# Kernel tuning notes

Hardware: AMD Instinct MI355X
Metric: run time of the kernel (lower is better)

## Reference

```python
import jax, jax.numpy as jnp
import numpy as np

N_NODES = 100000
N_EDGES = 600000
DIM = 128
LN_EPS = 1e-5


def setup_inputs() -> dict:
    key = jax.random.key(0)
    ks = jax.random.split(key, 12)
    s = 1.0 / np.sqrt(DIM)
    return {
        "h": jax.random.normal(ks[0], (N_NODES, DIM), dtype=jnp.float32),
        "edge_src": jax.random.randint(ks[1], (N_EDGES,), 0, N_NODES, dtype=jnp.int32),
        "edge_dst": jax.random.randint(ks[2], (N_EDGES,), 0, N_NODES, dtype=jnp.int32),
        "W_self": jax.random.uniform(ks[3], (DIM, DIM), jnp.float32, -s, s),
        "b_self": jax.random.uniform(ks[4], (DIM,), jnp.float32, -s, s),
        "W_neigh": jax.random.uniform(ks[5], (DIM, DIM), jnp.float32, -s, s),
        "b_neigh": jax.random.uniform(ks[6], (DIM,), jnp.float32, -s, s),
        "W_gate": jax.random.uniform(ks[7], (DIM, 2 * DIM), jnp.float32, -s, s),
        "b_gate": jax.random.uniform(ks[8], (DIM,), jnp.float32, -s, s),
        "ln_gamma": jnp.ones((DIM,), jnp.float32),
        "ln_beta": jnp.zeros((DIM,), jnp.float32),
    }


def reference(h, edge_src, edge_dst, W_self, b_self, W_neigh, b_neigh, W_gate, b_gate, ln_gamma, ln_beta):
    n = h.shape[0]
    # self transform: [N, D]
    hs = h @ W_self.T + b_self
    # mean over predecessors via segment sum over edges (src -> dst)
    neigh_sum = jax.ops.segment_sum(h[edge_src], edge_dst, num_segments=n)
    counts = jax.ops.segment_sum(jnp.ones((edge_src.shape[0],), h.dtype), edge_dst, num_segments=n)
    has_pred = (counts > 0).astype(h.dtype)[:, None]
    neigh_mean = neigh_sum / jnp.maximum(counts, 1.0)[:, None]
    hn = neigh_mean @ W_neigh.T + b_neigh
    # nodes with no predecessors skip the neighbor term entirely (incl. bias)
    m = hs + has_pred * hn
    gate = jax.nn.sigmoid(jnp.concatenate([h, m], axis=-1) @ W_gate.T + b_gate)
    v = gate * m + (1.0 - gate) * h
    # LayerNorm (biased variance, as torch) + relu
    mu = jnp.mean(v, axis=-1, keepdims=True)
    var = jnp.mean(jnp.square(v - mu), axis=-1, keepdims=True)
    out = (v - mu) * jax.lax.rsqrt(var + LN_EPS) * ln_gamma + ln_beta
    return jax.nn.relu(out)
```

## Files before the change

kernel.cpp:

```cpp
#include <hip/hip_runtime.h>
#include <math.h>

#define N_NODES 100000
#define N_EDGES 600000
#define DIM 128
#define LN_EPS 1e-5f
#define SCAN_NBLK ((N_NODES + 255) / 256)
#define NTILES ((N_NODES + 127) / 128)
#define NODE_GRID 256

typedef __bf16 bf16x8 __attribute__((ext_vector_type(8)));
typedef __bf16 bf16x4 __attribute__((ext_vector_type(4)));
typedef float f32x4 __attribute__((ext_vector_type(4)));

__global__ __launch_bounds__(256)
void prep_kernel(const float* __restrict__ h, const int* __restrict__ edst,
                 __bf16* __restrict__ h_bf, int* __restrict__ counts) {
  int i = blockIdx.x * 256 + threadIdx.x;
  {
    const float4 v0 = *reinterpret_cast<const float4*>(h + (size_t)i * 8);
    const float4 v1 = *reinterpret_cast<const float4*>(h + (size_t)i * 8 + 4);
    bf16x8 b;
    b[0] = (__bf16)v0.x; b[1] = (__bf16)v0.y; b[2] = (__bf16)v0.z; b[3] = (__bf16)v0.w;
    b[4] = (__bf16)v1.x; b[5] = (__bf16)v1.y; b[6] = (__bf16)v1.z; b[7] = (__bf16)v1.w;
    *reinterpret_cast<bf16x8*>(h_bf + (size_t)i * 8) = b;
  }
  if (i < N_EDGES) atomicAdd(&counts[edst[i]], 1);
}

__global__ __launch_bounds__(256)
void scan1_kernel(const int* __restrict__ counts, int* __restrict__ block_sums) {
  int i = blockIdx.x * 256 + threadIdx.x;
  int v = (i < N_NODES) ? counts[i] : 0;
#pragma unroll
  for (int off = 1; off < 64; off <<= 1) v += __shfl_xor(v, off);
  __shared__ int ws[4];
  if ((threadIdx.x & 63) == 0) ws[threadIdx.x >> 6] = v;
  __syncthreads();
  if (threadIdx.x == 0) block_sums[blockIdx.x] = ws[0] + ws[1] + ws[2] + ws[3];
}

__global__ __launch_bounds__(256)
void scan3_kernel(const int* __restrict__ counts, const int* __restrict__ block_sums,
                  int* __restrict__ row_off, int* __restrict__ cursor) {
  const int i = blockIdx.x * 256 + threadIdx.x;
  const int t = threadIdx.x;
  const int lane = t & 63, wv = t >> 6;
  __shared__ int wtot[4];
  __shared__ int sbase[4];

  int partial = 0;
  for (int j = t; j < blockIdx.x; j += 256) partial += block_sums[j];
#pragma unroll
  for (int off = 1; off < 64; off <<= 1) partial += __shfl_xor(partial, off);
  if (lane == 0) sbase[wv] = partial;
  __syncthreads();
  const int base = sbase[0] + sbase[1] + sbase[2] + sbase[3];

  int v = (i < N_NODES) ? counts[i] : 0;
  int s = v;
#pragma unroll
  for (int off = 1; off < 64; off <<= 1) {
    int u = __shfl_up(s, off);
    if (lane >= off) s += u;
  }
  if (lane == 63) wtot[wv] = s;
  __syncthreads();
  int wo = 0;
  for (int w = 0; w < wv; ++w) wo += wtot[w];
  int excl = base + wo + (s - v);
  if (i < N_NODES) { row_off[i] = excl; cursor[i] = 0; }
  if (i == 0) row_off[N_NODES] = N_EDGES;
}

__global__ __launch_bounds__(256)
void csr_fill_kernel(const int* __restrict__ esrc, const int* __restrict__ edst,
                     const int* __restrict__ row_off, int* __restrict__ cursor,
                     int* __restrict__ csr_src) {
  int base = (blockIdx.x * 256 + threadIdx.x) * 4;
  if (base >= N_EDGES) return;
  int4 s4 = *reinterpret_cast<const int4*>(esrc + base);
  int4 d4 = *reinterpret_cast<const int4*>(edst + base);
  {
    int pos = atomicAdd(&cursor[d4.x], 1);
    csr_src[row_off[d4.x] + pos] = s4.x;
  }
  {
    int pos = atomicAdd(&cursor[d4.y], 1);
    csr_src[row_off[d4.y] + pos] = s4.y;
  }
  {
    int pos = atomicAdd(&cursor[d4.z], 1);
    csr_src[row_off[d4.z] + pos] = s4.z;
  }
  {
    int pos = atomicAdd(&cursor[d4.w], 1);
    csr_src[row_off[d4.w] + pos] = s4.w;
  }
}

__global__ __launch_bounds__(256)
void gather_kernel(const __bf16* __restrict__ h_bf, const int* __restrict__ csr_src,
                   const int* __restrict__ row_off, __bf16* __restrict__ mean_bf) {
  int node = blockIdx.x * 16 + (threadIdx.x >> 4);
  if (node >= N_NODES) return;
  int t = threadIdx.x & 15;
  int b = row_off[node], e = row_off[node + 1];
  float acc[8];
#pragma unroll
  for (int j = 0; j < 8; ++j) acc[j] = 0.f;
  for (int i = b; i < e; i += 8) {
    int idx[8];
#pragma unroll
    for (int j = 0; j < 8; ++j) idx[j] = (i + j < e) ? csr_src[i + j] : -1;
    bf16x8 v[8];
#pragma unroll
    for (int j = 0; j < 8; ++j) {
      if (idx[j] >= 0)
        v[j] = *reinterpret_cast<const bf16x8*>(h_bf + (size_t)idx[j] * DIM + t * 8);
      else
#pragma unroll
        for (int k = 0; k < 8; ++k) v[j][k] = (__bf16)0.f;
    }
#pragma unroll
    for (int j = 0; j < 8; ++j)
#pragma unroll
      for (int k = 0; k < 8; ++k) acc[k] += (float)v[j][k];
  }
  float inv = (e > b) ? 1.0f / (float)(e - b) : 0.0f;
  bf16x8 mv;
#pragma unroll
  for (int j = 0; j < 8; ++j) mv[j] = (__bf16)(acc[j] * inv);
  *reinterpret_cast<bf16x8*>(mean_bf + (size_t)node * DIM + t * 8) = mv;
}

__global__ __launch_bounds__(512, 1)
void node_kernel(const __bf16* __restrict__ h_bf,
                 const __bf16* __restrict__ mean_bf,
                 const int* __restrict__ counts,
                 const float* __restrict__ Wself,
                 const float* __restrict__ Wneigh,
                 const float* __restrict__ Wgate,
                 const float* __restrict__ b_self,
                 const float* __restrict__ b_neigh,
                 const float* __restrict__ b_gate,
                 const float* __restrict__ ln_g,
                 const float* __restrict__ ln_b,
                 float* __restrict__ out) {
  __shared__ __align__(16) char smem[163840];
  char* Wl = smem;

  const int tid = threadIdx.x;

  for (int c = tid; c < 8192; c += 512) {
    int mi = c >> 11;
    int w = c & 2047;
    int row = w >> 4, col8 = w & 15;
    const float* src;
    if (mi == 0)      src = Wself  + row * 128 + col8 * 8;
    else if (mi == 1) src = Wneigh + row * 128 + col8 * 8;
    else if (mi == 2) src = Wgate  + row * 256 + col8 * 8;
    else              src = Wgate  + row * 256 + 128 + col8 * 8;
    float4 v0 = *reinterpret_cast<const float4*>(src);
    float4 v1 = *reinterpret_cast<const float4*>(src + 4);
    bf16x8 b;
    b[0] = (__bf16)v0.x; b[1] = (__bf16)v0.y; b[2] = (__bf16)v0.z; b[3] = (__bf16)v0.w;
    b[4] = (__bf16)v1.x; b[5] = (__bf16)v1.y; b[6] = (__bf16)v1.z; b[7] = (__bf16)v1.w;
    int byte = (row * 256 + col8 * 16) ^ ((row & 7) << 4);
    *reinterpret_cast<bf16x8*>(Wl + mi * 32768 + byte) = b;
  }
  __syncthreads();

  const int lane = tid & 63;
  const int wave = tid >> 6;
  const int col = lane & 15;
  const int kb = (lane >> 4) << 3;
  const int rloc = (lane >> 4) << 2;
  char* Ms = smem + 131072 + wave * 4096;

  for (int tile = blockIdx.x; tile < NTILES; tile += NODE_GRID) {
    const int node0 = tile * 128;

    bf16x8 a_h[4], a_m[4];
    {
      int n_a = node0 + wave * 16 + col;
      if (n_a < N_NODES) {
#pragma unroll
        for (int k0 = 0; k0 < 4; ++k0) {
          int koff = k0 * 32 + kb;
          a_h[k0] = *reinterpret_cast<const bf16x8*>(h_bf + (size_t)n_a * DIM + koff);
          a_m[k0] = *reinterpret_cast<const bf16x8*>(mean_bf + (size_t)n_a * DIM + koff);
        }
      } else {
#pragma unroll
        for (int k0 = 0; k0 < 4; ++k0)
#pragma unroll
          for (int j = 0; j < 8; ++j) { a_h[k0][j] = (__bf16)0.f; a_m[k0][j] = (__bf16)0.f; }
      }
    }

    int4 c4 = *reinterpret_cast<const int4*>(counts + node0 + wave * 16 + rloc);
    float hp[4];
    {
      int nb0 = node0 + wave * 16 + rloc;
      hp[0] = (nb0 + 0 < N_NODES && c4.x > 0) ? 1.f : 0.f;
      hp[1] = (nb0 + 1 < N_NODES && c4.y > 0) ? 1.f : 0.f;
      hp[2] = (nb0 + 2 < N_NODES && c4.z > 0) ? 1.f : 0.f;
      hp[3] = (nb0 + 3 < N_NODES && c4.w > 0) ? 1.f : 0.f;
    }

    f32x4 sacc[8], nacc[8];
#pragma unroll
    for (int i = 0; i < 8; ++i) {
      sacc[i] = (f32x4){0.f, 0.f, 0.f, 0.f};
      nacc[i] = (f32x4){0.f, 0.f, 0.f, 0.f};
    }
#pragma unroll
    for (int k0 = 0; k0 < 4; ++k0) {
      int koff2 = (k0 * 32 + kb) * 2;
#pragma unroll
      for (int nb = 0; nb < 8; ++nb) {
        int row = nb * 16 + col;
        int swz = (row * 256 + koff2) ^ ((row & 7) << 4);
        bf16x8 bs = *reinterpret_cast<const bf16x8*>(Wl + swz);
        bf16x8 bn = *reinterpret_cast<const bf16x8*>(Wl + 32768 + swz);
        sacc[nb] = __builtin_amdgcn_mfma_f32_16x16x32_bf16(a_h[k0], bs, sacc[nb], 0, 0, 0);
        nacc[nb] = __builtin_amdgcn_mfma_f32_16x16x32_bf16(a_m[k0], bn, nacc[nb], 0, 0, 0);
      }
    }

#pragma unroll
    for (int nb = 0; nb < 8; ++nb) {
      int d = nb * 16 + col;
      float bs = b_self[d], bn = b_neigh[d];
#pragma unroll
      for (int r = 0; r < 4; ++r) {
        float mval = sacc[nb][r] + bs + hp[r] * (nacc[nb][r] + bn);
        sacc[nb][r] = mval;
        int rl = rloc + r;
        int byte = (rl * 256 + d * 2) ^ ((rl & 7) << 4);
        *reinterpret_cast<__bf16*>(Ms + byte) = (__bf16)mval;
      }
    }

    f32x4 gacc[8];
#pragma unroll
    for (int i = 0; i < 8; ++i) gacc[i] = (f32x4){0.f, 0.f, 0.f, 0.f};
#pragma unroll
    for (int k0 = 0; k0 < 4; ++k0) {
      int koff2 = (k0 * 32 + kb) * 2;
      int abyte = (col * 256 + koff2) ^ ((col & 7) << 4);
      bf16x8 am2 = *reinterpret_cast<const bf16x8*>(Ms + abyte);
#pragma unroll
      for (int nb = 0; nb < 8; ++nb) {
        int row = nb * 16 + col;
        int swz = (row * 256 + koff2) ^ ((row & 7) << 4);
        bf16x8 bgh = *reinterpret_cast<const bf16x8*>(Wl + 65536 + swz);
        bf16x8 bgm = *reinterpret_cast<const bf16x8*>(Wl + 98304 + swz);
        gacc[nb] = __builtin_amdgcn_mfma_f32_16x16x32_bf16(a_h[k0], bgh, gacc[nb], 0, 0, 0);
        gacc[nb] = __builtin_amdgcn_mfma_f32_16x16x32_bf16(am2, bgm, gacc[nb], 0, 0, 0);
      }
    }

#pragma unroll
    for (int k0 = 0; k0 < 4; ++k0) {
      int byte = (col * 256 + (k0 * 32 + kb) * 2) ^ ((col & 7) << 4);
      *reinterpret_cast<bf16x8*>(Ms + byte) = a_h[k0];
    }

    float s1[4] = {0.f, 0.f, 0.f, 0.f}, s2[4] = {0.f, 0.f, 0.f, 0.f};
#pragma unroll
    for (int nb = 0; nb < 8; ++nb) {
      int d = nb * 16 + col;
      float bg = b_gate[d];
#pragma unroll
      for (int r = 0; r < 4; ++r) {
        int rl = rloc + r;
        int byte = (rl * 256 + d * 2) ^ ((rl & 7) << 4);
        float hval = (float)*reinterpret_cast<const __bf16*>(Ms + byte);
        float g = 1.0f / (1.0f + __expf(-(gacc[nb][r] + bg)));
        float v = g * sacc[nb][r] + (1.0f - g) * hval;
        s1[r] += v;
        s2[r] += v * v;
        *reinterpret_cast<__bf16*>(Ms + byte) = (__bf16)v;
      }
    }
#pragma unroll
    for (int off = 1; off < 16; off <<= 1) {
#pragma unroll
      for (int r = 0; r < 4; ++r) {
        s1[r] += __shfl_xor(s1[r], off);
        s2[r] += __shfl_xor(s2[r], off);
      }
    }
    float mu[4], rs[4];
#pragma unroll
    for (int r = 0; r < 4; ++r) {
      mu[r] = s1[r] * (1.0f / DIM);
      float var = s2[r] * (1.0f / DIM) - mu[r] * mu[r];
      rs[r] = rsqrtf(var + LN_EPS);
    }

    {
      int orow = lane >> 2;
      int ochunk = lane & 3;
      int gn = node0 + wave * 16 + orow;
      int rsel = orow & 3;
      float muv = (rsel & 2) ? ((rsel & 1) ? mu[3] : mu[2]) : ((rsel & 1) ? mu[1] : mu[0]);
      float rsv = (rsel & 2) ? ((rsel & 1) ? rs[3] : rs[2]) : ((rsel & 1) ? rs[1] : rs[0]);
      bool valid = gn < N_NODES;
#pragma unroll
      for (int j = 0; j < 4; ++j) {
        int d0 = ochunk * 8 + j * 32;
        int byte = (orow * 256 + d0 * 2) ^ ((orow & 7) << 4);
        bf16x8 vb = *reinterpret_cast<const bf16x8*>(Ms + byte);
        float4 g0 = *reinterpret_cast<const float4*>(ln_g + d0);
        float4 g1 = *reinterpret_cast<const float4*>(ln_g + d0 + 4);
        float4 e0 = *reinterpret_cast<const float4*>(ln_b + d0);
        float4 e1 = *reinterpret_cast<const float4*>(ln_b + d0 + 4);
        float4 o0, o1;
        o0.x = fmaxf(((float)vb[0] - muv) * rsv * g0.x + e0.x, 0.f);
        o0.y = fmaxf(((float)vb[1] - muv) * rsv * g0.y + e0.y, 0.f);
        o0.z = fmaxf(((float)vb[2] - muv) * rsv * g0.z + e0.z, 0.f);
        o0.w = fmaxf(((float)vb[3] - muv) * rsv * g0.w + e0.w, 0.f);
        o1.x = fmaxf(((float)vb[4] - muv) * rsv * g1.x + e1.x, 0.f);
        o1.y = fmaxf(((float)vb[5] - muv) * rsv * g1.y + e1.y, 0.f);
        o1.z = fmaxf(((float)vb[6] - muv) * rsv * g1.z + e1.z, 0.f);
        o1.w = fmaxf(((float)vb[7] - muv) * rsv * g1.w + e1.w, 0.f);
        if (valid) {
          *reinterpret_cast<float4*>(out + (size_t)gn * DIM + d0) = o0;
          *reinterpret_cast<float4*>(out + (size_t)gn * DIM + d0 + 4) = o1;
        }
      }
    }
  }
}

extern "C" void kernel_launch(void* const* d_in, const int* in_sizes, int n_in,
                              void* d_out, int out_size, void* d_ws, size_t ws_size,
                              hipStream_t stream) {
  const float* h      = (const float*)d_in[0];
  const int*   esrc   = (const int*)d_in[1];
  const int*   edst   = (const int*)d_in[2];
  const float* Wself  = (const float*)d_in[3];
  const float* bself  = (const float*)d_in[4];
  const float* Wneigh = (const float*)d_in[5];
  const float* bneigh = (const float*)d_in[6];
  const float* Wgate  = (const float*)d_in[7];
  const float* bgate  = (const float*)d_in[8];
  const float* ln_g   = (const float*)d_in[9];
  const float* ln_b   = (const float*)d_in[10];
  float* out = (float*)d_out;

  char* ws = (char*)d_ws;
  int* counts   = (int*)ws;
  int* row_off  = (int*)(ws + 400384);
  int* cursor   = (int*)(ws + 800768);
  int* csr_src  = (int*)(ws + 1200768);
  int* blk_sums = (int*)(ws + 3600768);
  __bf16* h_bf    = (__bf16*)(ws + 3602432);
  __bf16* mean_bf = (__bf16*)(ws + 29202432);

  hipMemsetAsync(counts, 0, (size_t)N_NODES * sizeof(int), stream);

  prep_kernel<<<6250, 256, 0, stream>>>(h, edst, h_bf, counts);
  scan1_kernel<<<SCAN_NBLK, 256, 0, stream>>>(counts, blk_sums);
  scan3_kernel<<<SCAN_NBLK, 256, 0, stream>>>(counts, blk_sums, row_off, cursor);
  csr_fill_kernel<<<(N_EDGES / 4 + 255) / 256, 256, 0, stream>>>(esrc, edst, row_off, cursor, csr_src);
  gather_kernel<<<(N_NODES + 15) / 16, 256, 0, stream>>>(h_bf, csr_src, row_off, mean_bf);
  node_kernel<<<NODE_GRID, 512, 0, stream>>>(
      h_bf, mean_bf, counts, Wself, Wneigh, Wgate,
      bself, bneigh, bgate, ln_g, ln_b, out);
}
```

Measured before the change: 154.3 us.

## Split fused node kernel into separate m and gate/LayerNorm kernels

The single node kernel, which held all four weight matrices in 160KB of LDS at one block per CU, is split in two. The first kernel computes m = self + neighbour transforms and writes it as bf16 in place over the mean buffer. The second loads only the gate weights, computes gate, mix and LayerNorm in the A-operand layout, and writes the output. This is meant to lower LDS and register pressure so more blocks fit per CU, on a larger grid. The cost is an extra kernel launch and an extra round-trip of m through global memory, and the gate sum now uses a bf16-rounded m.

```diff
diff --git a/kernel.cpp b/kernel.cpp
--- a/kernel.cpp
+++ b/kernel.cpp
@@ -7,7 +7,7 @@
 #define LN_EPS 1e-5f
 #define SCAN_NBLK ((N_NODES + 255) / 256)
 #define NTILES ((N_NODES + 127) / 128)
-#define NODE_GRID 256
+#define MG_GRID 512
 
 typedef __bf16 bf16x8 __attribute__((ext_vector_type(8)));
 typedef __bf16 bf16x4 __attribute__((ext_vector_type(4)));
@@ -134,33 +134,23 @@
   *reinterpret_cast<bf16x8*>(mean_bf + (size_t)node * DIM + t * 8) = mv;
 }
 
-__global__ __launch_bounds__(512, 1)
-void node_kernel(const __bf16* __restrict__ h_bf,
-                 const __bf16* __restrict__ mean_bf,
-                 const int* __restrict__ counts,
-                 const float* __restrict__ Wself,
-                 const float* __restrict__ Wneigh,
-                 const float* __restrict__ Wgate,
-                 const float* __restrict__ b_self,
-                 const float* __restrict__ b_neigh,
-                 const float* __restrict__ b_gate,
-                 const float* __restrict__ ln_g,
-                 const float* __restrict__ ln_b,
-                 float* __restrict__ out) {
-  __shared__ __align__(16) char smem[163840];
+__global__ __launch_bounds__(512, 4)
+void m_kernel(const __bf16* __restrict__ h_bf,
+              __bf16* __restrict__ mm_bf,
+              const int* __restrict__ counts,
+              const float* __restrict__ Wself,
+              const float* __restrict__ Wneigh,
+              const float* __restrict__ b_self,
+              const float* __restrict__ b_neigh) {
+  __shared__ __align__(16) char smem[65536];
   char* Wl = smem;
-
   const int tid = threadIdx.x;
 
-  for (int c = tid; c < 8192; c += 512) {
+  for (int c = tid; c < 4096; c += 512) {
     int mi = c >> 11;
     int w = c & 2047;
     int row = w >> 4, col8 = w & 15;
-    const float* src;
-    if (mi == 0)      src = Wself  + row * 128 + col8 * 8;
-    else if (mi == 1) src = Wneigh + row * 128 + col8 * 8;
-    else if (mi == 2) src = Wgate  + row * 256 + col8 * 8;
-    else              src = Wgate  + row * 256 + 128 + col8 * 8;
+    const float* src = (mi == 0 ? Wself : Wneigh) + row * 128 + col8 * 8;
     float4 v0 = *reinterpret_cast<const float4*>(src);
     float4 v1 = *reinterpret_cast<const float4*>(src + 4);
     bf16x8 b;
@@ -176,9 +166,8 @@
   const int col = lane & 15;
   const int kb = (lane >> 4) << 3;
   const int rloc = (lane >> 4) << 2;
-  char* Ms = smem + 131072 + wave * 4096;
-
-  for (int tile = blockIdx.x; tile < NTILES; tile += NODE_GRID) {
+
+  for (int tile = blockIdx.x; tile < NTILES; tile += MG_GRID) {
     const int node0 = tile * 128;
 
     bf16x8 a_h[4], a_m[4];
@@ -189,7 +178,7 @@
         for (int k0 = 0; k0 < 4; ++k0) {
           int koff = k0 * 32 + kb;
           a_h[k0] = *reinterpret_cast<const bf16x8*>(h_bf + (size_t)n_a * DIM + koff);
-          a_m[k0] = *reinterpret_cast<const bf16x8*>(mean_bf + (size_t)n_a * DIM + koff);
+          a_m[k0] = *reinterpret_cast<const bf16x8*>(mm_bf + (size_t)n_a * DIM + koff);
         }
       } else {
 #pragma unroll
@@ -229,6 +218,7 @@
       }
     }
 
+    const int nrow0 = node0 + wave * 16 + rloc;
 #pragma unroll
     for (int nb = 0; nb < 8; ++nb) {
       int d = nb * 16 + col;
@@ -236,10 +226,65 @@
 #pragma unroll
       for (int r = 0; r < 4; ++r) {
         float mval = sacc[nb][r] + bs + hp[r] * (nacc[nb][r] + bn);
-        sacc[nb][r] = mval;
-        int rl = rloc + r;
-        int byte = (rl * 256 + d * 2) ^ ((rl & 7) << 4);
-        *reinterpret_cast<__bf16*>(Ms + byte) = (__bf16)mval;
+        int n = nrow0 + r;
+        if (n < N_NODES) mm_bf[(size_t)n * DIM + d] = (__bf16)mval;
+      }
+    }
+  }
+}
+
+__global__ __launch_bounds__(512, 4)
+void g_kernel(const __bf16* __restrict__ h_bf,
+              const __bf16* __restrict__ m_bf,
+              const float* __restrict__ Wgate,
+              const float* __restrict__ b_gate,
+              const float* __restrict__ ln_g,
+              const float* __restrict__ ln_b,
+              float* __restrict__ out) {
+  __shared__ __align__(16) char smem[81920];
+  char* Wl = smem;
+  const int tid = threadIdx.x;
+
+  for (int c = tid; c < 4096; c += 512) {
+    int mi = c >> 11;
+    int w = c & 2047;
+    int row = w >> 4, col8 = w & 15;
+    const float* src = Wgate + row * 256 + mi * 128 + col8 * 8;
+    float4 v0 = *reinterpret_cast<const float4*>(src);
+    float4 v1 = *reinterpret_cast<const float4*>(src + 4);
+    bf16x8 b;
+    b[0] = (__bf16)v0.x; b[1] = (__bf16)v0.y; b[2] = (__bf16)v0.z; b[3] = (__bf16)v0.w;
+    b[4] = (__bf16)v1.x; b[5] = (__bf16)v1.y; b[6] = (__bf16)v1.z; b[7] = (__bf16)v1.w;
+    int byte = (row * 256 + col8 * 16) ^ ((row & 7) << 4);
+    *reinterpret_cast<bf16x8*>(Wl + mi * 32768 + byte) = b;
+  }
+  __syncthreads();
+
+  const int lane = tid & 63;
+  const int wave = tid >> 6;
+  const int col = lane & 15;
+  const int kb = (lane >> 4) << 3;
+  const int rloc = (lane >> 4) << 2;
+  char* St = smem + 65536 + wave * 2048;
+
+  for (int tile = blockIdx.x; tile < NTILES; tile += MG_GRID) {
+    const int node0 = tile * 128;
+
+    bf16x8 a_h[4], a_m[4];
+    {
+      int n_a = node0 + wave * 16 + col;
+      if (n_a < N_NODES) {
+#pragma unroll
+        for (int k0 = 0; k0 < 4; ++k0) {
+          int koff = k0 * 32 + kb;
+          a_h[k0] = *reinterpret_cast<const bf16x8*>(h_bf + (size_t)n_a * DIM + koff);
+          a_m[k0] = *reinterpret_cast<const bf16x8*>(m_bf + (size_t)n_a * DIM + koff);
+        }
+      } else {
+#pragma unroll
+        for (int k0 = 0; k0 < 4; ++k0)
+#pragma unroll
+          for (int j = 0; j < 8; ++j) { a_h[k0][j] = (__bf16)0.f; a_m[k0][j] = (__bf16)0.f; }
       }
     }
 
@@ -249,87 +294,85 @@
 #pragma unroll
     for (int k0 = 0; k0 < 4; ++k0) {
       int koff2 = (k0 * 32 + kb) * 2;
-      int abyte = (col * 256 + koff2) ^ ((col & 7) << 4);
-      bf16x8 am2 = *reinterpret_cast<const bf16x8*>(Ms + abyte);
 #pragma unroll
       for (int nb = 0; nb < 8; ++nb) {
         int row = nb * 16 + col;
         int swz = (row * 256 + koff2) ^ ((row & 7) << 4);
-        bf16x8 bgh = *reinterpret_cast<const bf16x8*>(Wl + 65536 + swz);
-        bf16x8 bgm = *reinterpret_cast<const bf16x8*>(Wl + 98304 + swz);
+        bf16x8 bgh = *reinterpret_cast<const bf16x8*>(Wl + swz);
+        bf16x8 bgm = *reinterpret_cast<const bf16x8*>(Wl + 32768 + swz);
         gacc[nb] = __builtin_amdgcn_mfma_f32_16x16x32_bf16(a_h[k0], bgh, gacc[nb], 0, 0, 0);
-        gacc[nb] = __builtin_amdgcn_mfma_f32_16x16x32_bf16(am2, bgm, gacc[nb], 0, 0, 0);
-      }
-    }
-
+        gacc[nb] = __builtin_amdgcn_mfma_f32_16x16x32_bf16(a_m[k0], bgm, gacc[nb], 0, 0, 0);
+      }
+    }
+
+    bf16x8 gt[4];
+#pragma unroll
+    for (int half = 0; half < 2; ++half) {
+#pragma unroll
+      for (int nbl = 0; nbl < 4; ++nbl) {
+        int nb = half * 4 + nbl;
+        int offd = nb * 16 + col - half * 64;
+#pragma unroll
+        for (int r = 0; r < 4; ++r) {
+          int rl = rloc + r;
+          int byte = (rl * 128 + offd * 2) ^ ((rl & 7) << 4);
+          *reinterpret_cast<__bf16*>(St + byte) = (__bf16)gacc[nb][r];
+        }
+      }
+#pragma unroll
+      for (int kk = 0; kk < 2; ++kk) {
+        int k0 = half * 2 + kk;
+        int off = k0 * 32 + kb - half * 64;
+        int byte = (col * 128 + off * 2) ^ ((col & 7) << 4);
+        gt[k0] = *reinterpret_cast<const bf16x8*>(St + byte);
+      }
+    }
+
+    float s1 = 0.f, s2 = 0.f;
+    float vv[4][8];
 #pragma unroll
     for (int k0 = 0; k0 < 4; ++k0) {
-      int byte = (col * 256 + (k0 * 32 + kb) * 2) ^ ((col & 7) << 4);
-      *reinterpret_cast<bf16x8*>(Ms + byte) = a_h[k0];
-    }
-
-    float s1[4] = {0.f, 0.f, 0.f, 0.f}, s2[4] = {0.f, 0.f, 0.f, 0.f};
-#pragma unroll
-    for (int nb = 0; nb < 8; ++nb) {
-      int d = nb * 16 + col;
-      float bg = b_gate[d];
-#pragma unroll
-      for (int r = 0; r < 4; ++r) {
-        int rl = rloc + r;
-        int byte = (rl * 256 + d * 2) ^ ((rl & 7) << 4);
-        float hval = (float)*reinterpret_cast<const __bf16*>(Ms + byte);
-        float g = 1.0f / (1.0f + __expf(-(gacc[nb][r] + bg)));
-        float v = g * sacc[nb][r] + (1.0f - g) * hval;
-        s1[r] += v;
-        s2[r] += v * v;
-        *reinterpret_cast<__bf16*>(Ms + byte) = (__bf16)v;
-      }
-    }
-#pragma unroll
-    for (int off = 1; off < 16; off <<= 1) {
-#pragma unroll
-      for (int r = 0; r < 4; ++r) {
-        s1[r] += __shfl_xor(s1[r], off);
-        s2[r] += __shfl_xor(s2[r], off);
-      }
-    }
-    float mu[4], rs[4];
-#pragma unroll
-    for (int r = 0; r < 4; ++r) {
-      mu[r] = s1[r] * (1.0f / DIM);
-      float var = s2[r] * (1.0f / DIM) - mu[r] * mu[r];
-      rs[r] = rsqrtf(var + LN_EPS);
-    }
+      int c0 = k0 * 32 + kb;
+      float4 bg0 = *reinterpret_cast<const float4*>(b_gate + c0);
+      float4 bg1 = *reinterpret_cast<const float4*>(b_gate + c0 + 4);
+      float bgv[8] = {bg0.x, bg0.y, bg0.z, bg0.w, bg1.x, bg1.y, bg1.z, bg1.w};
+#pragma unroll
+      for (int j = 0; j < 8; ++j) {
+        float g = 1.0f / (1.0f + __expf(-((float)gt[k0][j] + bgv[j])));
+        float v = g * (float)a_m[k0][j] + (1.0f - g) * (float)a_h[k0][j];
+        vv[k0][j] = v;
+        s1 += v;
+        s2 += v * v;
+      }
+    }
+    s1 += __shfl_xor(s1, 16); s1 += __shfl_xor(s1, 32);
+    s2 += __shfl_xor(s2, 16); s2 += __shfl_xor(s2, 32);
+    float mu = s1 * (1.0f / DIM);
+    float var = s2 * (1.0f / DIM) - mu * mu;
+    float rs = rsqrtf(var + LN_EPS);
 
     {
-      int orow = lane >> 2;
-      int ochunk = lane & 3;
-      int gn = node0 + wave * 16 + orow;
-      int rsel = orow & 3;
-      float muv = (rsel & 2) ? ((rsel & 1) ? mu[3] : mu[2]) : ((rsel & 1) ? mu[1] : mu[0]);
-      float rsv = (rsel & 2) ? ((rsel & 1) ? rs[3] : rs[2]) : ((rsel & 1) ? rs[1] : rs[0]);
+      int gn = node0 + wave * 16 + col;
       bool valid = gn < N_NODES;
 #pragma unroll
-      for (int j = 0; j < 4; ++j) {
-        int d0 = ochunk * 8 + j * 32;
-        int byte = (orow * 256 + d0 * 2) ^ ((orow & 7) << 4);
-        bf16x8 vb = *reinterpret_cast<const bf16x8*>(Ms + byte);
-        float4 g0 = *reinterpret_cast<const float4*>(ln_g + d0);
-        float4 g1 = *reinterpret_cast<const float4*>(ln_g + d0 + 4);
-        float4 e0 = *reinterpret_cast<const float4*>(ln_b + d0);
-        float4 e1 = *reinterpret_cast<const float4*>(ln_b + d0 + 4);
+      for (int k0 = 0; k0 < 4; ++k0) {
+        int c0 = k0 * 32 + kb;
+        float4 g0 = *reinterpret_cast<const float4*>(ln_g + c0);
+        float4 g1 = *reinterpret_cast<const float4*>(ln_g + c0 + 4);
+        float4 e0 = *reinterpret_cast<const float4*>(ln_b + c0);
+        float4 e1 = *reinterpret_cast<const float4*>(ln_b + c0 + 4);
         float4 o0, o1;
-        o0.x = fmaxf(((float)vb[0] - muv) * rsv * g0.x + e0.x, 0.f);
-        o0.y = fmaxf(((float)vb[1] - muv) * rsv * g0.y + e0.y, 0.f);
-        o0.z = fmaxf(((float)vb[2] - muv) * rsv * g0.z + e0.z, 0.f);
-        o0.w = fmaxf(((float)vb[3] - muv) * rsv * g0.w + e0.w, 0.f);
-        o1.x = fmaxf(((float)vb[4] - muv) * rsv * g1.x + e1.x, 0.f);
-        o1.y = fmaxf(((float)vb[5] - muv) * rsv * g1.y + e1.y, 0.f);
-        o1.z = fmaxf(((float)vb[6] - muv) * rsv * g1.z + e1.z, 0.f);
-        o1.w = fmaxf(((float)vb[7] - muv) * rsv * g1.w + e1.w, 0.f);
+        o0.x = fmaxf((vv[k0][0] - mu) * rs * g0.x + e0.x, 0.f);
+        o0.y = fmaxf((vv[k0][1] - mu) * rs * g0.y + e0.y, 0.f);
+        o0.z = fmaxf((vv[k0][2] - mu) * rs * g0.z + e0.z, 0.f);
+        o0.w = fmaxf((vv[k0][3] - mu) * rs * g0.w + e0.w, 0.f);
+        o1.x = fmaxf((vv[k0][4] - mu) * rs * g1.x + e1.x, 0.f);
+        o1.y = fmaxf((vv[k0][5] - mu) * rs * g1.y + e1.y, 0.f);
+        o1.z = fmaxf((vv[k0][6] - mu) * rs * g1.z + e1.z, 0.f);
+        o1.w = fmaxf((vv[k0][7] - mu) * rs * g1.w + e1.w, 0.f);
         if (valid) {
-          *reinterpret_cast<float4*>(out + (size_t)gn * DIM + d0) = o0;
-          *reinterpret_cast<float4*>(out + (size_t)gn * DIM + d0 + 4) = o1;
+          *reinterpret_cast<float4*>(out + (size_t)gn * DIM + c0) = o0;
+          *reinterpret_cast<float4*>(out + (size_t)gn * DIM + c0 + 4) = o1;
         }
       }
     }
@@ -359,7 +402,7 @@
   int* csr_src  = (int*)(ws + 1200768);
   int* blk_sums = (int*)(ws + 3600768);
   __bf16* h_bf    = (__bf16*)(ws + 3602432);
-  __bf16* mean_bf = (__bf16*)(ws + 29202432);
+  __bf16* mm_bf   = (__bf16*)(ws + 29202432);
 
   hipMemsetAsync(counts, 0, (size_t)N_NODES * sizeof(int), stream);
 
@@ -367,8 +410,7 @@
   scan1_kernel<<<SCAN_NBLK, 256, 0, stream>>>(counts, blk_sums);
   scan3_kernel<<<SCAN_NBLK, 256, 0, stream>>>(counts, blk_sums, row_off, cursor);
   csr_fill_kernel<<<(N_EDGES / 4 + 255) / 256, 256, 0, stream>>>(esrc, edst, row_off, cursor, csr_src);
-  gather_kernel<<<(N_NODES + 15) / 16, 256, 0, stream>>>(h_bf, csr_src, row_off, mean_bf);
-  node_kernel<<<NODE_GRID, 512, 0, stream>>>(
-      h_bf, mean_bf, counts, Wself, Wneigh, Wgate,
-      bself, bneigh, bgate, ln_g, ln_b, out);
-}
+  gather_kernel<<<(N_NODES + 15) / 16, 256, 0, stream>>>(h_bf, csr_src, row_off, mm_bf);
+  m_kernel<<<MG_GRID, 512, 0, stream>>>(h_bf, mm_bf, counts, Wself, Wneigh, bself, bneigh);
+  g_kernel<<<MG_GRID, 512, 0, stream>>>(h_bf, mm_bf, Wgate, bgate, ln_g, ln_b, out);
+}
```

Measured after the change: 353.5 us. +129.1%, slower.

## Fuse neighbor-mean gather into node kernel, dropping intermediate mean buffer

Applied to the files above, without the earlier changes.

Removes the separate gather kernel and computes each node's neighbor mean directly in the node kernel's A-fragment load, walking CSR neighbors and accumulating bf16 rows in registers. This avoids writing and re-reading the bf16 mean array and one kernel launch. In exchange the irregular gather runs inside a low-occupancy persistent kernel with only two neighbors in flight per lane, which may expose memory latency.

```diff
diff --git a/kernel.cpp b/kernel.cpp
--- a/kernel.cpp
+++ b/kernel.cpp
@@ -99,44 +99,10 @@
   }
 }
 
-__global__ __launch_bounds__(256)
-void gather_kernel(const __bf16* __restrict__ h_bf, const int* __restrict__ csr_src,
-                   const int* __restrict__ row_off, __bf16* __restrict__ mean_bf) {
-  int node = blockIdx.x * 16 + (threadIdx.x >> 4);
-  if (node >= N_NODES) return;
-  int t = threadIdx.x & 15;
-  int b = row_off[node], e = row_off[node + 1];
-  float acc[8];
-#pragma unroll
-  for (int j = 0; j < 8; ++j) acc[j] = 0.f;
-  for (int i = b; i < e; i += 8) {
-    int idx[8];
-#pragma unroll
-    for (int j = 0; j < 8; ++j) idx[j] = (i + j < e) ? csr_src[i + j] : -1;
-    bf16x8 v[8];
-#pragma unroll
-    for (int j = 0; j < 8; ++j) {
-      if (idx[j] >= 0)
-        v[j] = *reinterpret_cast<const bf16x8*>(h_bf + (size_t)idx[j] * DIM + t * 8);
-      else
-#pragma unroll
-        for (int k = 0; k < 8; ++k) v[j][k] = (__bf16)0.f;
-    }
-#pragma unroll
-    for (int j = 0; j < 8; ++j)
-#pragma unroll
-      for (int k = 0; k < 8; ++k) acc[k] += (float)v[j][k];
-  }
-  float inv = (e > b) ? 1.0f / (float)(e - b) : 0.0f;
-  bf16x8 mv;
-#pragma unroll
-  for (int j = 0; j < 8; ++j) mv[j] = (__bf16)(acc[j] * inv);
-  *reinterpret_cast<bf16x8*>(mean_bf + (size_t)node * DIM + t * 8) = mv;
-}
-
 __global__ __launch_bounds__(512, 1)
 void node_kernel(const __bf16* __restrict__ h_bf,
-                 const __bf16* __restrict__ mean_bf,
+                 const int* __restrict__ row_off,
+                 const int* __restrict__ csr_src,
                  const int* __restrict__ counts,
                  const float* __restrict__ Wself,
                  const float* __restrict__ Wneigh,
@@ -180,23 +146,72 @@
 
   for (int tile = blockIdx.x; tile < NTILES; tile += NODE_GRID) {
     const int node0 = tile * 128;
-
-    bf16x8 a_h[4], a_m[4];
+    const int n_a = node0 + wave * 16 + col;
+    const bool va = n_a < N_NODES;
+
+    bf16x8 a_m[4];
     {
-      int n_a = node0 + wave * 16 + col;
-      if (n_a < N_NODES) {
-#pragma unroll
-        for (int k0 = 0; k0 < 4; ++k0) {
-          int koff = k0 * 32 + kb;
-          a_h[k0] = *reinterpret_cast<const bf16x8*>(h_bf + (size_t)n_a * DIM + koff);
-          a_m[k0] = *reinterpret_cast<const bf16x8*>(mean_bf + (size_t)n_a * DIM + koff);
+      int b = 0, e = 0;
+      if (va) { b = row_off[n_a]; e = row_off[n_a + 1]; }
+      float m0[8], m1[8], m2[8], m3[8];
+#pragma unroll
+      for (int j = 0; j < 8; ++j) { m0[j] = 0.f; m1[j] = 0.f; m2[j] = 0.f; m3[j] = 0.f; }
+      int i = b;
+      for (; i + 2 <= e; i += 2) {
+        int s0 = csr_src[i], s1 = csr_src[i + 1];
+        const __bf16* r0 = h_bf + (size_t)s0 * DIM + kb;
+        const __bf16* r1 = h_bf + (size_t)s1 * DIM + kb;
+        bf16x8 u0 = *reinterpret_cast<const bf16x8*>(r0);
+        bf16x8 u1 = *reinterpret_cast<const bf16x8*>(r0 + 32);
+        bf16x8 u2 = *reinterpret_cast<const bf16x8*>(r0 + 64);
+        bf16x8 u3 = *reinterpret_cast<const bf16x8*>(r0 + 96);
+        bf16x8 w0 = *reinterpret_cast<const bf16x8*>(r1);
+        bf16x8 w1 = *reinterpret_cast<const bf16x8*>(r1 + 32);
+        bf16x8 w2 = *reinterpret_cast<const bf16x8*>(r1 + 64);
+        bf16x8 w3 = *reinterpret_cast<const bf16x8*>(r1 + 96);
+#pragma unroll
+        for (int j = 0; j < 8; ++j) {
+          m0[j] += (float)u0[j] + (float)w0[j];
+          m1[j] += (float)u1[j] + (float)w1[j];
+          m2[j] += (float)u2[j] + (float)w2[j];
+          m3[j] += (float)u3[j] + (float)w3[j];
         }
-      } else {
-#pragma unroll
-        for (int k0 = 0; k0 < 4; ++k0)
-#pragma unroll
-          for (int j = 0; j < 8; ++j) { a_h[k0][j] = (__bf16)0.f; a_m[k0][j] = (__bf16)0.f; }
-      }
+      }
+      if (i < e) {
+        int s0 = csr_src[i];
+        const __bf16* r0 = h_bf + (size_t)s0 * DIM + kb;
+        bf16x8 u0 = *reinterpret_cast<const bf16x8*>(r0);
+        bf16x8 u1 = *reinterpret_cast<const bf16x8*>(r0 + 32);
+        bf16x8 u2 = *reinterpret_cast<const bf16x8*>(r0 + 64);
+        bf16x8 u3 = *reinterpret_cast<const bf16x8*>(r0 + 96);
+#pragma unroll
+        for (int j = 0; j < 8; ++j) {
+          m0[j] += (float)u0[j];
+          m1[j] += (float)u1[j];
+          m2[j] += (float)u2[j];
+          m3[j] += (float)u3[j];
+        }
+      }
+      float inv = (e > b) ? 1.0f / (float)(e - b) : 0.0f;
+#pragma unroll
+      for (int j = 0; j < 8; ++j) {
+        a_m[0][j] = (__bf16)(m0[j] * inv);
+        a_m[1][j] = (__bf16)(m1[j] * inv);
+        a_m[2][j] = (__bf16)(m2[j] * inv);
+        a_m[3][j] = (__bf16)(m3[j] * inv);
+      }
+    }
+
+    bf16x8 a_h[4];
+    if (va) {
+#pragma unroll
+      for (int k0 = 0; k0 < 4; ++k0)
+        a_h[k0] = *reinterpret_cast<const bf16x8*>(h_bf + (size_t)n_a * DIM + k0 * 32 + kb);
+    } else {
+#pragma unroll
+      for (int k0 = 0; k0 < 4; ++k0)
+#pragma unroll
+        for (int j = 0; j < 8; ++j) a_h[k0][j] = (__bf16)0.f;
     }
 
     int4 c4 = *reinterpret_cast<const int4*>(counts + node0 + wave * 16 + rloc);
@@ -358,8 +373,7 @@
   int* cursor   = (int*)(ws + 800768);
   int* csr_src  = (int*)(ws + 1200768);
   int* blk_sums = (int*)(ws + 3600768);
-  __bf16* h_bf    = (__bf16*)(ws + 3602432);
-  __bf16* mean_bf = (__bf16*)(ws + 29202432);
+  __bf16* h_bf  = (__bf16*)(ws + 3602432);
 
   hipMemsetAsync(counts, 0, (size_t)N_NODES * sizeof(int), stream);
 
@@ -367,8 +381,7 @@
   scan1_kernel<<<SCAN_NBLK, 256, 0, stream>>>(counts, blk_sums);
   scan3_kernel<<<SCAN_NBLK, 256, 0, stream>>>(counts, blk_sums, row_off, cursor);
   csr_fill_kernel<<<(N_EDGES / 4 + 255) / 256, 256, 0, stream>>>(esrc, edst, row_off, cursor, csr_src);
-  gather_kernel<<<(N_NODES + 15) / 16, 256, 0, stream>>>(h_bf, csr_src, row_off, mean_bf);
   node_kernel<<<NODE_GRID, 512, 0, stream>>>(
-      h_bf, mean_bf, counts, Wself, Wneigh, Wgate,
+      h_bf, row_off, csr_src, counts, Wself, Wneigh, Wgate,
       bself, bneigh, bgate, ln_g, ln_b, out);
 }
```

Measured after the change: 157.4 us. 1.02x slower.
